# Optimization experiments

Measured on AMD Instinct MI355X. Metric: run time of the kernel, lower is better.

## Reference

```python
import jax, jax.numpy as jnp
import numpy as np
from jax import lax

# pywt db4 decomposition lowpass filter
_DEC_LO_NP = np.array([-0.010597401784997278, 0.032883011666982945,
                        0.030841381835986965, -0.18703481171888114,
                        -0.02798376941698385, 0.6308807679295904,
                        0.7148465705525415, 0.23037781330885523], dtype=np.float32)
_SIGNS = np.array([(-1.0) ** (k + 1) for k in range(8)], dtype=np.float32)
DEC_LO = jnp.asarray(_DEC_LO_NP)                    # dec_lo
DEC_HI = jnp.asarray(_DEC_LO_NP[::-1] * _SIGNS)     # dec_hi (QMF)
LF = 8
MAX_LEVEL = 4
# analysis kernels: torch cross-correlates with reversed dec filters == true conv
H_ANA = jnp.stack([DEC_LO[::-1], DEC_HI[::-1]])[:, None, :]  # (2,1,LF)
# synthesis: torch conv_transpose with rec filters == xcorr(dilated x, flip(rec)) = xcorr with dec
G0F = DEC_LO[None, None, :]
G1F = DEC_HI[None, None, :]
DN = ('NCH', 'OIH', 'NCH')


def _dwt_step(x):
    # x: (N, Lx) -> (lo, hi) each (N, outsize); pytorch_wavelets afb1d, mode='symmetric'
    N = x.shape[-1]
    outsize = (N + LF - 1) // 2          # pywt.dwt_coeff_len
    p = 2 * (outsize - 1) - N + LF
    xp = jnp.pad(x, ((0, 0), (p // 2, (p + 1) // 2)), mode='symmetric')
    y = lax.conv_general_dilated(xp[:, None, :], H_ANA, (2,), 'VALID',
                                 dimension_numbers=DN)  # (N,2,outsize)
    return y[:, 0, :], y[:, 1, :]


def _idwt_step(lo, hi):
    # pytorch_wavelets sfb1d: conv_transpose(stride=2, padding=LF-2)
    # == lhs-dilated xcorr with flipped rec filters (= dec filters), pad 1 each side
    y0 = lax.conv_general_dilated(lo[:, None, :], G0F, (1,), [(1, 1)],
                                  lhs_dilation=(2,), dimension_numbers=DN)
    y1 = lax.conv_general_dilated(hi[:, None, :], G1F, (1,), [(1, 1)],
                                  lhs_dilation=(2,), dimension_numbers=DN)
    return (y0 + y1)[:, 0, :]            # (N, 2*Llo + 2 - LF)


def dywpe(x, proj_w, proj_b, scale_emb, gate_w, gate_b):
    B, L, _ = x.shape
    d_model = scale_emb.shape[1]
    # channel_proj -> mono signal (B, L)
    x_mono = (jnp.einsum('blc,oc->blo', x, proj_w) + proj_b)[..., 0]
    # multi-level DWT
    lo = x_mono
    highs = []
    for _ in range(MAX_LEVEL):
        lo, hi = _dwt_step(lo)
        highs.append(hi)
    # gates: sigmoid(g) * tanh(v), per scale -> (MAX_LEVEL+1, d_model)
    gated = scale_emb @ gate_w.T + gate_b
    g, v = jnp.split(gated, 2, axis=-1)
    gates = jax.nn.sigmoid(g) * jnp.tanh(v)

    def mod(coef, gate):  # (B,Lc) x (d,) -> (B*d, Lc): outer product, fold d into batch
        return (coef[:, None, :] * gate[None, :, None]).reshape(B * d_model, -1)

    x0 = mod(lo, gates[0])
    hs = [mod(highs[i], gates[i + 1]) for i in range(MAX_LEVEL)]
    # IDWT, coarsest level first
    for h in hs[::-1]:
        if x0.shape[-1] > h.shape[-1]:
            x0 = x0[:, :h.shape[-1]]
        x0 = _idwt_step(x0, h)
    pe = x0.reshape(B, d_model, -1).transpose(0, 2, 1)  # (B, L', d_model)
    if pe.shape[1] < L:
        pe = jnp.pad(pe, ((0, 0), (0, L - pe.shape[1]), (0, 0)))
    elif pe.shape[1] > L:
        pe = pe[:, :L]
    return pe


def setup_inputs() -> dict:
    key = jax.random.key(0)
    ks = jax.random.split(key, 6)
    B, L, d_x, d_model, J = 32, 4096, 8, 512, 4
    return {
        'x': jax.random.normal(ks[0], (B, L, d_x), dtype=jnp.float32),
        'proj_w': jax.random.normal(ks[1], (1, d_x), dtype=jnp.float32) * 0.3,
        'proj_b': jax.random.normal(ks[2], (1,), dtype=jnp.float32) * 0.02,
        'scale_emb': jax.random.normal(ks[3], (J + 1, d_model), dtype=jnp.float32),
        'gate_w': jax.random.normal(ks[4], (2 * d_model, d_model), dtype=jnp.float32) * 0.04,
        'gate_b': jax.random.normal(ks[5], (2 * d_model,), dtype=jnp.float32) * 0.02,
    }


def reference(x, proj_w, proj_b, scale_emb, gate_w, gate_b):
    return dywpe(x, proj_w, proj_b, scale_emb, gate_w, gate_b)
```

## Files before the change

kernel.cpp:

```cpp
#include <hip/hip_runtime.h>

#define NB    32
#define LSEQ  4096
#define DM    512
#define WROWS 32
#define BROWS 128
#define NBLK  (NB * LSEQ / BROWS)

typedef float f32x4 __attribute__((ext_vector_type(4)));

__device__ __constant__ float c_DL[8] = {
    -0.010597401784997278f,  0.032883011666982945f,  0.030841381835986965f,
    -0.18703481171888114f,  -0.02798376941698385f,   0.6308807679295904f,
     0.7148465705525415f,    0.23037781330885523f};
__device__ __constant__ float c_DH[8] = {
    -0.23037781330885523f,   0.7148465705525415f,   -0.6308807679295904f,
    -0.02798376941698385f,   0.18703481171888114f,   0.030841381835986965f,
    -0.032883011666982945f, -0.010597401784997278f};

#define O_XW   0
#define O_LO1  240
#define O_LO2  360
#define O_LO3  416
#define O_HI1  440
#define O_H2   460
#define O_H3   476
#define O_L4   488
#define O_H4   498
#define O_A    508
#define O_A4   520
#define O_A3   532
#define O_B    548
#define O_B4   564
#define O_P0   580
#define O_P2   600
#define O_P3   620
#define O_P4   640
#define CONE_STRIDE 672

__device__ __forceinline__ int imin(int a, int b) { return a < b ? a : b; }
__device__ __forceinline__ int imax(int a, int b) { return a > b ? a : b; }

__device__ __forceinline__ int reflect_idx(int i, int N) {
    if (i < 0)  i = -1 - i;
    if (i >= N) i = 2 * N - 1 - i;
    return i;
}

template <bool HI>
__device__ void fwd_range_w(const float* __restrict__ src, int src_lo, int Nsrc,
                            float* __restrict__ dst, int d_lo, int d_hi, int lane) {
    for (int t = d_lo + lane; t <= d_hi; t += 64) {
        int base = 2 * t - 6;
        float acc = 0.f;
#pragma unroll
        for (int k = 0; k < 8; ++k) {
            float xv = src[reflect_idx(base + k, Nsrc) - src_lo];
            acc = fmaf(xv, HI ? c_DH[7 - k] : c_DL[7 - k], acc);
        }
        dst[t - d_lo] = acc;
    }
}

template <bool HI>
__device__ void inv_range_w(const float* __restrict__ c, int c_lo,
                            float* __restrict__ y, int y_lo, int y_hi, int lane) {
    for (int t = y_lo + lane; t <= y_hi; t += 64) {
        int base = (t >> 1) - c_lo;
        int odd = t & 1;
        float f0 = odd ? (HI ? c_DH[0] : c_DL[0]) : (HI ? c_DH[1] : c_DL[1]);
        float f1 = odd ? (HI ? c_DH[2] : c_DL[2]) : (HI ? c_DH[3] : c_DL[3]);
        float f2 = odd ? (HI ? c_DH[4] : c_DL[4]) : (HI ? c_DH[5] : c_DL[5]);
        float f3 = odd ? (HI ? c_DH[6] : c_DL[6]) : (HI ? c_DH[7] : c_DL[7]);
        float acc = c[base] * f0;
        acc = fmaf(c[base + 1], f1, acc);
        acc = fmaf(c[base + 2], f2, acc);
        acc = fmaf(c[base + 3], f3, acc);
        y[t - y_lo] = acc;
    }
}

__global__ __launch_bounds__(1024) void gates_kernel(
    const float* __restrict__ scale_emb, const float* __restrict__ gate_w,
    const float* __restrict__ gate_b, float* __restrict__ gates) {
    int lane = threadIdx.x & 63;
    int c = blockIdx.x * 16 + (threadIdx.x >> 6);
    const float4* rg = (const float4*)(gate_w + (size_t)c * DM) + lane * 2;
    const float4* rv = (const float4*)(gate_w + (size_t)(c + DM) * DM) + lane * 2;
    float4 a0 = rg[0], a1 = rg[1];
    float4 b0 = rv[0], b1 = rv[1];
    float gacc[5], vacc[5];
#pragma unroll
    for (int j = 0; j < 5; ++j) {
        const float4* sj = (const float4*)(scale_emb + (size_t)j * DM) + lane * 2;
        float4 s0 = sj[0], s1 = sj[1];
        float ga;
        ga = s0.x * a0.x;            ga = fmaf(s0.y, a0.y, ga);
        ga = fmaf(s0.z, a0.z, ga);   ga = fmaf(s0.w, a0.w, ga);
        ga = fmaf(s1.x, a1.x, ga);   ga = fmaf(s1.y, a1.y, ga);
        ga = fmaf(s1.z, a1.z, ga);   ga = fmaf(s1.w, a1.w, ga);
        float va;
        va = s0.x * b0.x;            va = fmaf(s0.y, b0.y, va);
        va = fmaf(s0.z, b0.z, va);   va = fmaf(s0.w, b0.w, va);
        va = fmaf(s1.x, b1.x, va);   va = fmaf(s1.y, b1.y, va);
        va = fmaf(s1.z, b1.z, va);   va = fmaf(s1.w, b1.w, va);
        gacc[j] = ga;
        vacc[j] = va;
    }
#pragma unroll
    for (int j = 0; j < 5; ++j) {
#pragma unroll
        for (int off = 32; off > 0; off >>= 1) {
            gacc[j] += __shfl_xor(gacc[j], off, 64);
            vacc[j] += __shfl_xor(vacc[j], off, 64);
        }
    }
    if (lane == 0) {
        float bg = gate_b[c], bv = gate_b[DM + c];
#pragma unroll
        for (int j = 0; j < 5; ++j) {
            float g = gacc[j] + bg;
            float v = vacc[j] + bv;
            float sg = 1.f / (1.f + expf(-g));
            gates[j * DM + c] = sg * tanhf(v);
        }
    }
}

__global__ __launch_bounds__(256, 4) void fused_kernel(
    const float* __restrict__ x, const float* __restrict__ proj_w,
    const float* __restrict__ proj_b, const float* __restrict__ gates,
    float* __restrict__ out) {
    __shared__ float GL[5 * DM];
    __shared__ float CB[4][CONE_STRIDE];
    __shared__ float SJ[5 * BROWS];

    int bid = blockIdx.x;
    int b  = bid >> 5;
    int l0 = (bid & 31) * BROWS;
    int wid = threadIdx.x >> 6;
    int lane = threadIdx.x & 63;
    int l0w = l0 + wid * WROWS;

    for (int i = threadIdx.x; i < 5 * DM / 4; i += 256)
        ((f32x4*)GL)[i] = ((const f32x4*)gates)[i];

    int p0 = l0w >> 1,  p1 = ((l0w + WROWS - 1) >> 1) + 3;
    int b0 = p0 >> 1,   b1 = (p1 >> 1) + 3;
    int a0 = b0 >> 1,   a1 = (b1 >> 1) + 3;
    int w0 = a0 >> 1,   w1 = (a1 >> 1) + 3;
    int t3lo = imax(imin(imin(2 * w0 - 6, a0), 517), 0);
    int t3hi = imin(imax(imax(2 * w1 + 1, a1), 0), 517);
    int t2lo = imax(imin(2 * t3lo - 6, 2 * a0 - 6), 0);
    int t2hi = imin(imax(2 * t3hi + 1, 2 * a1 + 1), 1028);
    int t1lo = imax(imin(2 * t2lo - 6, 2 * b0 - 6), 0);
    int t1hi = imin(imax(2 * t2hi + 1, 2 * b1 + 1), 2050);
    int txlo = imax(imin(2 * t1lo - 6, 2 * p0 - 6), 0);
    int txhi = imin(imax(2 * t1hi + 1, 2 * p1 + 1), 4095);

    float* W = CB[wid];

    {
        float w[8];
#pragma unroll
        for (int k = 0; k < 8; ++k) w[k] = proj_w[k];
        float pb = proj_b[0];
        const float* xb = x + (size_t)b * LSEQ * 8;
        for (int i = txlo + lane; i <= txhi; i += 64) {
            const float4* xv = (const float4*)(xb + (size_t)i * 8);
            float4 q0 = xv[0], q1 = xv[1];
            float acc = pb;
            acc = fmaf(q0.x, w[0], acc); acc = fmaf(q0.y, w[1], acc);
            acc = fmaf(q0.z, w[2], acc); acc = fmaf(q0.w, w[3], acc);
            acc = fmaf(q1.x, w[4], acc); acc = fmaf(q1.y, w[5], acc);
            acc = fmaf(q1.z, w[6], acc); acc = fmaf(q1.w, w[7], acc);
            W[O_XW + i - txlo] = acc;
        }
    }

    fwd_range_w<false>(W + O_XW, txlo, 4096, W + O_LO1, t1lo, t1hi, lane);
    fwd_range_w<true >(W + O_XW, txlo, 4096, W + O_HI1, p0, p1, lane);
    fwd_range_w<false>(W + O_LO1, t1lo, 2051, W + O_LO2, t2lo, t2hi, lane);
    fwd_range_w<true >(W + O_LO1, t1lo, 2051, W + O_H2, b0, b1, lane);
    fwd_range_w<false>(W + O_LO2, t2lo, 1029, W + O_LO3, t3lo, t3hi, lane);
    fwd_range_w<true >(W + O_LO2, t2lo, 1029, W + O_H3, a0, a1, lane);
    fwd_range_w<false>(W + O_LO3, t3lo, 518, W + O_L4, w0, w1, lane);
    fwd_range_w<true >(W + O_LO3, t3lo, 518, W + O_H4, w0, w1, lane);

    inv_range_w<false>(W + O_L4, w0, W + O_A,  a0, a1, lane);
    inv_range_w<true >(W + O_H4, w0, W + O_A4, a0, a1, lane);
    inv_range_w<true >(W + O_H3, a0, W + O_A3, b0, b1, lane);
    inv_range_w<true >(W + O_H2, b0, W + O_P2, p0, p1, lane);
    inv_range_w<false>(W + O_A,  a0, W + O_B,  b0, b1, lane);
    inv_range_w<false>(W + O_A4, a0, W + O_B4, b0, b1, lane);
    inv_range_w<false>(W + O_A3, b0, W + O_P3, p0, p1, lane);
    inv_range_w<false>(W + O_B,  b0, W + O_P0, p0, p1, lane);
    inv_range_w<false>(W + O_B4, b0, W + O_P4, p0, p1, lane);

    for (int idx = lane; idx < 5 * WROWS; idx += 64) {
        int j = idx >> 5;
        int r = idx & (WROWS - 1);
        int l = l0w + r;
        int base = (l >> 1) - p0;
        int odd = l & 1;
        const float* Pj = (j == 0) ? (W + O_P0) : (j == 1) ? (W + O_HI1) :
                          (j == 2) ? (W + O_P2) : (j == 3) ? (W + O_P3) : (W + O_P4);
        bool hi = (j == 1);
        float f0 = odd ? (hi ? c_DH[0] : c_DL[0]) : (hi ? c_DH[1] : c_DL[1]);
        float f1 = odd ? (hi ? c_DH[2] : c_DL[2]) : (hi ? c_DH[3] : c_DL[3]);
        float f2 = odd ? (hi ? c_DH[4] : c_DL[4]) : (hi ? c_DH[5] : c_DL[5]);
        float f3 = odd ? (hi ? c_DH[6] : c_DL[6]) : (hi ? c_DH[7] : c_DL[7]);
        float acc = Pj[base] * f0;
        acc = fmaf(Pj[base + 1], f1, acc);
        acc = fmaf(Pj[base + 2], f2, acc);
        acc = fmaf(Pj[base + 3], f3, acc);
        SJ[j * BROWS + wid * WROWS + r] = acc;
    }
    __syncthreads();

    int half = threadIdx.x >> 7;
    int c4 = threadIdx.x & 127;
    f32x4 g0 = ((const f32x4*)(GL + 0 * DM))[c4];
    f32x4 g1 = ((const f32x4*)(GL + 1 * DM))[c4];
    f32x4 g2 = ((const f32x4*)(GL + 2 * DM))[c4];
    f32x4 g3 = ((const f32x4*)(GL + 3 * DM))[c4];
    f32x4 g4 = ((const f32x4*)(GL + 4 * DM))[c4];

    size_t rowbase = (size_t)b * LSEQ + l0;
#pragma unroll 4
    for (int r = 0; r < BROWS / 2; ++r) {
        int rr = r * 2 + half;
        float s0 = SJ[rr];
        float s1 = SJ[BROWS + rr];
        float s2 = SJ[2 * BROWS + rr];
        float s3 = SJ[3 * BROWS + rr];
        float s4 = SJ[4 * BROWS + rr];
        f32x4 acc;
        acc.x = fmaf(s4, g4.x, fmaf(s3, g3.x, fmaf(s2, g2.x, fmaf(s1, g1.x, s0 * g0.x))));
        acc.y = fmaf(s4, g4.y, fmaf(s3, g3.y, fmaf(s2, g2.y, fmaf(s1, g1.y, s0 * g0.y))));
        acc.z = fmaf(s4, g4.z, fmaf(s3, g3.z, fmaf(s2, g2.z, fmaf(s1, g1.z, s0 * g0.z))));
        acc.w = fmaf(s4, g4.w, fmaf(s3, g3.w, fmaf(s2, g2.w, fmaf(s1, g1.w, s0 * g0.w))));
        __builtin_nontemporal_store(acc, (f32x4*)out + (rowbase + rr) * (DM / 4) + c4);
    }
}

extern "C" void kernel_launch(void* const* d_in, const int* in_sizes, int n_in,
                              void* d_out, int out_size, void* d_ws, size_t ws_size,
                              hipStream_t stream) {
    const float* x         = (const float*)d_in[0];
    const float* proj_w    = (const float*)d_in[1];
    const float* proj_b    = (const float*)d_in[2];
    const float* scale_emb = (const float*)d_in[3];
    const float* gate_w    = (const float*)d_in[4];
    const float* gate_b    = (const float*)d_in[5];
    float* out   = (float*)d_out;
    float* gates = (float*)d_ws;

    gates_kernel<<<32, 1024, 0, stream>>>(scale_emb, gate_w, gate_b, gates);
    fused_kernel<<<NBLK, 256, 0, stream>>>(x, proj_w, proj_b, gates, out);
}
```

Measured before the change: 66.30 us.

## Split wavelet cone computation from output expansion and co-schedule gate computation

Restructures the pipeline so a first kernel computes the per-level reconstructed coefficient arrays (P-level signals) once per batch in 32-wide half-resolution chunks, with the gate GEMV folded into extra blocks of the same launch. A second kernel reads gates and the P arrays from workspace and writes the large (B, L, 512) output with many small blocks. The aim is to cut the redundant overlapping cone recomputation per 32-row warp and to run the gates work alongside the cone work instead of as a separate serial launch. In exchange it adds a global-memory round trip for the intermediate coefficients.

```diff
diff --git a/kernel.cpp b/kernel.cpp
--- a/kernel.cpp
+++ b/kernel.cpp
@@ -3,11 +3,17 @@
 #define NB    32
 #define LSEQ  4096
 #define DM    512
-#define WROWS 32
-#define BROWS 128
-#define NBLK  (NB * LSEQ / BROWS)
 
 typedef float f32x4 __attribute__((ext_vector_type(4)));
+
+#define GATES_OFF 0
+#define P_OFF     (5 * DM)
+#define P_STRIDE  2052
+
+#define CH_PER_B    65
+#define NTASK       (NB * CH_PER_B)
+#define PROD_BLOCKS ((NTASK + 3) / 4)
+#define GATE_BLOCKS 128
 
 __device__ __constant__ float c_DL[8] = {
     -0.010597401784997278f,  0.032883011666982945f,  0.030841381835986965f,
@@ -19,24 +25,24 @@
     -0.032883011666982945f, -0.010597401784997278f};
 
 #define O_XW   0
-#define O_LO1  240
-#define O_LO2  360
-#define O_LO3  416
-#define O_HI1  440
-#define O_H2   460
-#define O_H3   476
-#define O_L4   488
-#define O_H4   498
-#define O_A    508
-#define O_A4   520
-#define O_A3   532
-#define O_B    548
-#define O_B4   564
-#define O_P0   580
-#define O_P2   600
-#define O_P3   620
-#define O_P4   640
-#define CONE_STRIDE 672
+#define O_LO1  280
+#define O_LO2  424
+#define O_LO3  496
+#define O_HI1  536
+#define O_H2   576
+#define O_H3   604
+#define O_L4   624
+#define O_H4   640
+#define O_A    656
+#define O_A4   676
+#define O_A3   696
+#define O_B    724
+#define O_B4   752
+#define O_P0   772
+#define O_P2   812
+#define O_P3   852
+#define O_P4   892
+#define CONE_STRIDE 928
 
 __device__ __forceinline__ int imin(int a, int b) { return a < b ? a : b; }
 __device__ __forceinline__ int imax(int a, int b) { return a > b ? a : b; }
@@ -80,75 +86,70 @@
     }
 }
 
-__global__ __launch_bounds__(1024) void gates_kernel(
-    const float* __restrict__ scale_emb, const float* __restrict__ gate_w,
-    const float* __restrict__ gate_b, float* __restrict__ gates) {
-    int lane = threadIdx.x & 63;
-    int c = blockIdx.x * 16 + (threadIdx.x >> 6);
-    const float4* rg = (const float4*)(gate_w + (size_t)c * DM) + lane * 2;
-    const float4* rv = (const float4*)(gate_w + (size_t)(c + DM) * DM) + lane * 2;
-    float4 a0 = rg[0], a1 = rg[1];
-    float4 b0 = rv[0], b1 = rv[1];
-    float gacc[5], vacc[5];
-#pragma unroll
-    for (int j = 0; j < 5; ++j) {
-        const float4* sj = (const float4*)(scale_emb + (size_t)j * DM) + lane * 2;
-        float4 s0 = sj[0], s1 = sj[1];
-        float ga;
-        ga = s0.x * a0.x;            ga = fmaf(s0.y, a0.y, ga);
-        ga = fmaf(s0.z, a0.z, ga);   ga = fmaf(s0.w, a0.w, ga);
-        ga = fmaf(s1.x, a1.x, ga);   ga = fmaf(s1.y, a1.y, ga);
-        ga = fmaf(s1.z, a1.z, ga);   ga = fmaf(s1.w, a1.w, ga);
-        float va;
-        va = s0.x * b0.x;            va = fmaf(s0.y, b0.y, va);
-        va = fmaf(s0.z, b0.z, va);   va = fmaf(s0.w, b0.w, va);
-        va = fmaf(s1.x, b1.x, va);   va = fmaf(s1.y, b1.y, va);
-        va = fmaf(s1.z, b1.z, va);   va = fmaf(s1.w, b1.w, va);
-        gacc[j] = ga;
-        vacc[j] = va;
-    }
-#pragma unroll
-    for (int j = 0; j < 5; ++j) {
-#pragma unroll
-        for (int off = 32; off > 0; off >>= 1) {
-            gacc[j] += __shfl_xor(gacc[j], off, 64);
-            vacc[j] += __shfl_xor(vacc[j], off, 64);
-        }
-    }
-    if (lane == 0) {
-        float bg = gate_b[c], bv = gate_b[DM + c];
-#pragma unroll
-        for (int j = 0; j < 5; ++j) {
-            float g = gacc[j] + bg;
-            float v = vacc[j] + bv;
-            float sg = 1.f / (1.f + expf(-g));
-            gates[j * DM + c] = sg * tanhf(v);
-        }
-    }
-}
-
-__global__ __launch_bounds__(256, 4) void fused_kernel(
+__global__ __launch_bounds__(256, 4) void prod_gates_kernel(
     const float* __restrict__ x, const float* __restrict__ proj_w,
-    const float* __restrict__ proj_b, const float* __restrict__ gates,
-    float* __restrict__ out) {
-    __shared__ float GL[5 * DM];
-    __shared__ float CB[4][CONE_STRIDE];
-    __shared__ float SJ[5 * BROWS];
-
-    int bid = blockIdx.x;
-    int b  = bid >> 5;
-    int l0 = (bid & 31) * BROWS;
+    const float* __restrict__ proj_b, const float* __restrict__ scale_emb,
+    const float* __restrict__ gate_w, const float* __restrict__ gate_b,
+    float* __restrict__ ws) {
     int wid = threadIdx.x >> 6;
     int lane = threadIdx.x & 63;
-    int l0w = l0 + wid * WROWS;
-
-    for (int i = threadIdx.x; i < 5 * DM / 4; i += 256)
-        ((f32x4*)GL)[i] = ((const f32x4*)gates)[i];
-
-    int p0 = l0w >> 1,  p1 = ((l0w + WROWS - 1) >> 1) + 3;
-    int b0 = p0 >> 1,   b1 = (p1 >> 1) + 3;
-    int a0 = b0 >> 1,   a1 = (b1 >> 1) + 3;
-    int w0 = a0 >> 1,   w1 = (a1 >> 1) + 3;
+
+    if (blockIdx.x >= PROD_BLOCKS) {
+        int c = (blockIdx.x - PROD_BLOCKS) * 4 + wid;
+        const float4* rg = (const float4*)(gate_w + (size_t)c * DM) + lane * 2;
+        const float4* rv = (const float4*)(gate_w + (size_t)(c + DM) * DM) + lane * 2;
+        float4 a0 = rg[0], a1 = rg[1];
+        float4 b0 = rv[0], b1 = rv[1];
+        float gacc[5], vacc[5];
+#pragma unroll
+        for (int j = 0; j < 5; ++j) {
+            const float4* sj = (const float4*)(scale_emb + (size_t)j * DM) + lane * 2;
+            float4 s0 = sj[0], s1 = sj[1];
+            float ga;
+            ga = s0.x * a0.x;            ga = fmaf(s0.y, a0.y, ga);
+            ga = fmaf(s0.z, a0.z, ga);   ga = fmaf(s0.w, a0.w, ga);
+            ga = fmaf(s1.x, a1.x, ga);   ga = fmaf(s1.y, a1.y, ga);
+            ga = fmaf(s1.z, a1.z, ga);   ga = fmaf(s1.w, a1.w, ga);
+            float va;
+            va = s0.x * b0.x;            va = fmaf(s0.y, b0.y, va);
+            va = fmaf(s0.z, b0.z, va);   va = fmaf(s0.w, b0.w, va);
+            va = fmaf(s1.x, b1.x, va);   va = fmaf(s1.y, b1.y, va);
+            va = fmaf(s1.z, b1.z, va);   va = fmaf(s1.w, b1.w, va);
+            gacc[j] = ga;
+            vacc[j] = va;
+        }
+#pragma unroll
+        for (int j = 0; j < 5; ++j) {
+#pragma unroll
+            for (int off = 32; off > 0; off >>= 1) {
+                gacc[j] += __shfl_xor(gacc[j], off, 64);
+                vacc[j] += __shfl_xor(vacc[j], off, 64);
+            }
+        }
+        if (lane == 0) {
+            float bg = gate_b[c], bv = gate_b[DM + c];
+#pragma unroll
+            for (int j = 0; j < 5; ++j) {
+                float g = gacc[j] + bg;
+                float v = vacc[j] + bv;
+                float sg = 1.f / (1.f + expf(-g));
+                ws[GATES_OFF + j * DM + c] = sg * tanhf(v);
+            }
+        }
+        return;
+    }
+
+    __shared__ float CB[4][CONE_STRIDE];
+    int task = blockIdx.x * 4 + wid;
+    if (task >= NTASK) return;
+    int b  = task / CH_PER_B;
+    int cc = task % CH_PER_B;
+    int p0 = cc * 32;
+    int p1 = imin(p0 + 31, 2050);
+
+    int b0 = p0 >> 1,  b1 = (p1 >> 1) + 3;
+    int a0 = b0 >> 1,  a1 = (b1 >> 1) + 3;
+    int w0 = a0 >> 1,  w1 = (a1 >> 1) + 3;
     int t3lo = imax(imin(imin(2 * w0 - 6, a0), 517), 0);
     int t3hi = imin(imax(imax(2 * w1 + 1, a1), 0), 517);
     int t2lo = imax(imin(2 * t3lo - 6, 2 * a0 - 6), 0);
@@ -197,15 +198,37 @@
     inv_range_w<false>(W + O_B,  b0, W + O_P0, p0, p1, lane);
     inv_range_w<false>(W + O_B4, b0, W + O_P4, p0, p1, lane);
 
-    for (int idx = lane; idx < 5 * WROWS; idx += 64) {
-        int j = idx >> 5;
-        int r = idx & (WROWS - 1);
-        int l = l0w + r;
-        int base = (l >> 1) - p0;
+    float* P = ws + P_OFF;
+    for (int t = p0 + lane; t <= p1; t += 64) {
+        int o = t - p0;
+        P[(size_t)(0 * NB + b) * P_STRIDE + t] = W[O_P0 + o];
+        P[(size_t)(1 * NB + b) * P_STRIDE + t] = W[O_HI1 + o];
+        P[(size_t)(2 * NB + b) * P_STRIDE + t] = W[O_P2 + o];
+        P[(size_t)(3 * NB + b) * P_STRIDE + t] = W[O_P3 + o];
+        P[(size_t)(4 * NB + b) * P_STRIDE + t] = W[O_P4 + o];
+    }
+}
+
+__global__ __launch_bounds__(256) void expand_kernel(
+    const float* __restrict__ ws, float* __restrict__ out) {
+    const float* gates = ws + GATES_OFF;
+    __shared__ float gl[5 * DM];
+    __shared__ float sArr[5 * 32];
+    for (int i = threadIdx.x; i < 5 * DM / 4; i += 256)
+        ((f32x4*)gl)[i] = ((const f32x4*)gates)[i];
+
+    int bid = blockIdx.x;
+    int b  = bid >> 7;
+    int l0 = (bid & 127) * 32;
+
+    int t = threadIdx.x;
+    if (t < 160) {
+        int j = t >> 5, r = t & 31;
+        int l = l0 + r;
+        int base = l >> 1;
         int odd = l & 1;
-        const float* Pj = (j == 0) ? (W + O_P0) : (j == 1) ? (W + O_HI1) :
-                          (j == 2) ? (W + O_P2) : (j == 3) ? (W + O_P3) : (W + O_P4);
         bool hi = (j == 1);
+        const float* Pj = ws + P_OFF + (size_t)(j * NB + b) * P_STRIDE;
         float f0 = odd ? (hi ? c_DH[0] : c_DL[0]) : (hi ? c_DH[1] : c_DL[1]);
         float f1 = odd ? (hi ? c_DH[2] : c_DL[2]) : (hi ? c_DH[3] : c_DL[3]);
         float f2 = odd ? (hi ? c_DH[4] : c_DL[4]) : (hi ? c_DH[5] : c_DL[5]);
@@ -214,33 +237,33 @@
         acc = fmaf(Pj[base + 1], f1, acc);
         acc = fmaf(Pj[base + 2], f2, acc);
         acc = fmaf(Pj[base + 3], f3, acc);
-        SJ[j * BROWS + wid * WROWS + r] = acc;
+        sArr[t] = acc;
     }
     __syncthreads();
 
     int half = threadIdx.x >> 7;
     int c4 = threadIdx.x & 127;
-    f32x4 g0 = ((const f32x4*)(GL + 0 * DM))[c4];
-    f32x4 g1 = ((const f32x4*)(GL + 1 * DM))[c4];
-    f32x4 g2 = ((const f32x4*)(GL + 2 * DM))[c4];
-    f32x4 g3 = ((const f32x4*)(GL + 3 * DM))[c4];
-    f32x4 g4 = ((const f32x4*)(GL + 4 * DM))[c4];
-
-    size_t rowbase = (size_t)b * LSEQ + l0;
+    f32x4 g0 = ((const f32x4*)(gl + 0 * DM))[c4];
+    f32x4 g1 = ((const f32x4*)(gl + 1 * DM))[c4];
+    f32x4 g2 = ((const f32x4*)(gl + 2 * DM))[c4];
+    f32x4 g3 = ((const f32x4*)(gl + 3 * DM))[c4];
+    f32x4 g4 = ((const f32x4*)(gl + 4 * DM))[c4];
+
 #pragma unroll 4
-    for (int r = 0; r < BROWS / 2; ++r) {
+    for (int r = 0; r < 16; ++r) {
         int rr = r * 2 + half;
-        float s0 = SJ[rr];
-        float s1 = SJ[BROWS + rr];
-        float s2 = SJ[2 * BROWS + rr];
-        float s3 = SJ[3 * BROWS + rr];
-        float s4 = SJ[4 * BROWS + rr];
+        int row = bid * 32 + rr;
+        float s0 = sArr[rr];
+        float s1 = sArr[32 + rr];
+        float s2 = sArr[64 + rr];
+        float s3 = sArr[96 + rr];
+        float s4 = sArr[128 + rr];
         f32x4 acc;
         acc.x = fmaf(s4, g4.x, fmaf(s3, g3.x, fmaf(s2, g2.x, fmaf(s1, g1.x, s0 * g0.x))));
         acc.y = fmaf(s4, g4.y, fmaf(s3, g3.y, fmaf(s2, g2.y, fmaf(s1, g1.y, s0 * g0.y))));
         acc.z = fmaf(s4, g4.z, fmaf(s3, g3.z, fmaf(s2, g2.z, fmaf(s1, g1.z, s0 * g0.z))));
         acc.w = fmaf(s4, g4.w, fmaf(s3, g3.w, fmaf(s2, g2.w, fmaf(s1, g1.w, s0 * g0.w))));
-        __builtin_nontemporal_store(acc, (f32x4*)out + (rowbase + rr) * (DM / 4) + c4);
+        __builtin_nontemporal_store(acc, (f32x4*)out + (size_t)row * (DM / 4) + c4);
     }
 }
 
@@ -253,9 +276,10 @@
     const float* scale_emb = (const float*)d_in[3];
     const float* gate_w    = (const float*)d_in[4];
     const float* gate_b    = (const float*)d_in[5];
-    float* out   = (float*)d_out;
-    float* gates = (float*)d_ws;
-
-    gates_kernel<<<32, 1024, 0, stream>>>(scale_emb, gate_w, gate_b, gates);
-    fused_kernel<<<NBLK, 256, 0, stream>>>(x, proj_w, proj_b, gates, out);
-}
+    float* out = (float*)d_out;
+    float* ws  = (float*)d_ws;
+
+    prod_gates_kernel<<<PROD_BLOCKS + GATE_BLOCKS, 256, 0, stream>>>(
+        x, proj_w, proj_b, scale_emb, gate_w, gate_b, ws);
+    expand_kernel<<<(NB * LSEQ) / 32, 256, 0, stream>>>(ws, out);
+}
```

After: 70.28 us. 6.0% more time.
